# Optimization experiments

Measured on AMD Instinct MI355X. Metric: run time of the kernel, lower is better.

Reference implementation:

```python
import jax, jax.numpy as jnp
import numpy as np

B, T, HID, NH = 8, 4096, 768, 12
HD = HID // NH          # 64
WIN = 128 // 2          # half window = 64 (local_attention=128)
BLK = 64                # block size == half window
THETA = 10000.0         # local_rope_theta
ATTN_SCALING = 1.0      # default rope type


def setup_inputs() -> dict:
    key = jax.random.key(0)
    k1, k2, k3 = jax.random.split(key, 3)
    hidden_states = jax.random.normal(k1, (B, T, HID), jnp.float32)
    attention_mask = jnp.ones((B, T), jnp.bool_)
    Wqkv = jax.random.normal(k2, (3 * HID, HID), jnp.float32) * 0.02
    Wo = jax.random.normal(k3, (HID, HID), jnp.float32) * 0.02
    return {"hidden_states": hidden_states, "attention_mask": attention_mask,
            "Wqkv": Wqkv, "Wo": Wo}


def _rope(x):
    # x: [B, T, NH, HD]; interleaved-pair complex rotation (pairs = reshape(HD//2, 2))
    pos = jnp.arange(T, dtype=jnp.float32)
    inv_freq = 1.0 / (THETA ** (jnp.arange(0, HD, 2, dtype=jnp.float32) / HD))  # [HD/2]
    ang = pos[:, None] * inv_freq[None, :]                 # [T, HD/2]
    cos = jnp.cos(ang)[None, :, None, :]
    sin = jnp.sin(ang)[None, :, None, :]
    pairs = x.reshape(x.shape[:-1] + (HD // 2, 2))
    a, b = pairs[..., 0], pairs[..., 1]
    ra = a * cos - b * sin
    rb = a * sin + b * cos
    return (jnp.stack([ra, rb], axis=-1).reshape(x.shape)) * ATTN_SCALING


def reference(hidden_states, attention_mask, Wqkv, Wo):
    # fused QKV projection (no bias: attention_bias=False)
    qkv = hidden_states @ Wqkv.T                            # [B, T, 3*HID]
    qkv = qkv.reshape(B, T, 3, NH, HD)
    q, k, v = qkv[:, :, 0], qkv[:, :, 1], qkv[:, :, 2]      # [B, T, NH, HD]
    q = _rope(q)
    k = _rope(k)

    # Blocked sliding-window attention: block = 64, each query block attends
    # key blocks {i-1, i, i+1}; exact +/-64 band enforced by mask.
    nb = T // BLK
    pad = [(0, 0), (BLK, BLK), (0, 0), (0, 0)]
    kp = jnp.pad(k, pad)
    vp = jnp.pad(v, pad)
    kb = kp.reshape(B, nb + 2, BLK, NH, HD)
    vb = vp.reshape(B, nb + 2, BLK, NH, HD)
    knb = jnp.concatenate([kb[:, :-2], kb[:, 1:-1], kb[:, 2:]], axis=2)  # [B, nb, 3*BLK, NH, HD]
    vnb = jnp.concatenate([vb[:, :-2], vb[:, 1:-1], vb[:, 2:]], axis=2)
    qb = q.reshape(B, nb, BLK, NH, HD)

    scores = jnp.einsum('bnqhd,bnkhd->bhnqk', qb, knb) / jnp.sqrt(jnp.float32(HD))
    band = jnp.abs(BLK + jnp.arange(BLK)[:, None] - jnp.arange(3 * BLK)[None, :]) <= WIN  # [BLK, 3*BLK]
    mp = jnp.pad(attention_mask.astype(jnp.bool_), [(0, 0), (BLK, BLK)])
    mb = mp.reshape(B, nb + 2, BLK)
    mnb = jnp.concatenate([mb[:, :-2], mb[:, 1:-1], mb[:, 2:]], axis=2)  # [B, nb, 3*BLK]
    mask = band[None, None, None] & mnb[:, None, :, None, :]
    scores = jnp.where(mask, scores, -jnp.inf)
    probs = jax.nn.softmax(scores, axis=-1)
    out = jnp.einsum('bhnqk,bnkhd->bnqhd', probs, vnb)      # [B, nb, BLK, NH, HD]
    out = out.reshape(B, T, HID)
    return out @ Wo.T
```

## Files before the change

kernel.cpp:

```cpp
#include <hip/hip_runtime.h>
#include <hip/hip_bf16.h>

#define T_SEQ 4096
#define NH 12

typedef __bf16 bf16x8 __attribute__((ext_vector_type(8)));
typedef float f32x4 __attribute__((ext_vector_type(4)));
typedef unsigned int uint32;

__device__ __forceinline__ void gload_lds16(const void* g, void* lds) {
    __builtin_amdgcn_global_load_lds((const __attribute__((address_space(1))) void*)g,
                                     (__attribute__((address_space(3))) void*)lds,
                                     16, 0, 0);
}

__device__ __forceinline__ f32x4 mfma16(bf16x8 a, bf16x8 b, f32x4 c) {
    return __builtin_amdgcn_mfma_f32_16x16x32_bf16(a, b, c, 0, 0, 0);
}

__device__ __forceinline__ void store_out(__hip_bfloat16* p, float v) { *p = __float2bfloat16(v); }
__device__ __forceinline__ void store_out(float* p, float v) { *p = v; }

__global__ __launch_bounds__(256) void f32_to_bf16_kernel(const float* __restrict__ src,
                                                          __hip_bfloat16* __restrict__ dst,
                                                          long n8) {
    long i = (long)blockIdx.x * 256 + threadIdx.x;
    if (i >= n8) return;
    float4 a = *(const float4*)(src + i * 8);
    float4 b = *(const float4*)(src + i * 8 + 4);
    __hip_bfloat16 o[8];
    o[0] = __float2bfloat16(a.x); o[1] = __float2bfloat16(a.y);
    o[2] = __float2bfloat16(a.z); o[3] = __float2bfloat16(a.w);
    o[4] = __float2bfloat16(b.x); o[5] = __float2bfloat16(b.y);
    o[6] = __float2bfloat16(b.z); o[7] = __float2bfloat16(b.w);
    *(uint4*)(dst + i * 8) = *(uint4*)o;
}

__global__ void rope_table_kernel(float2* __restrict__ tab) {
    int idx = blockIdx.x * 256 + threadIdx.x;
    int tpos = idx >> 5, i = idx & 31;
    float invf = powf(10000.0f, -(2.0f * i) / 64.0f);
    float ang = (float)tpos * invf;
    tab[idx] = make_float2((float)cos((double)ang), (float)sin((double)ang));
}


#define PHASE(BB, MH, NH, SKIND, SKT, DOSTAGE)                                            \
    do {                                                                                  \
        bf16x8 af[4][2], bq[2][2];                                                        \
        _Pragma("unroll")                                                                 \
        for (int m2 = 0; m2 < 4; ++m2)                                                    \
            _Pragma("unroll")                                                             \
            for (int ks = 0; ks < 2; ++ks) {                                              \
                const int row = wr * 128 + ((MH) * 4 + m2) * 16 + li;                     \
                af[m2][ks] = *(const bf16x8*)((char*)&As[BB][0] + row * 128 +             \
                                              (((ks * 4 + g) ^ (row & 7)) << 4));         \
            }                                                                             \
        _Pragma("unroll")                                                                 \
        for (int n2 = 0; n2 < 2; ++n2)                                                    \
            _Pragma("unroll")                                                             \
            for (int ks = 0; ks < 2; ++ks) {                                              \
                const int row = wc * 64 + ((NH) * 2 + n2) * 16 + li;                      \
                bq[n2][ks] = *(const bf16x8*)((char*)&Bs[BB][0] + row * 128 +             \
                                              (((ks * 4 + g) ^ (row & 7)) << 4));         \
            }                                                                             \
        if (DOSTAGE) STAGE_HT((SKIND), (SKT));                                            \
        __builtin_amdgcn_sched_barrier(0);                                                \
        __builtin_amdgcn_s_barrier();                                                     \
        __builtin_amdgcn_s_setprio(1);                                                    \
        _Pragma("unroll")                                                                 \
        for (int m2 = 0; m2 < 4; ++m2)                                                    \
            _Pragma("unroll")                                                             \
            for (int n2 = 0; n2 < 2; ++n2)                                                \
                _Pragma("unroll")                                                         \
                for (int ks = 0; ks < 2; ++ks)                                            \
                    acc[(MH) * 4 + m2][(NH) * 2 + n2] =                                   \
                        mfma16(af[m2][ks], bq[n2][ks], acc[(MH) * 4 + m2][(NH) * 2 + n2]);\
        __builtin_amdgcn_s_setprio(0);                                                    \
        __builtin_amdgcn_sched_barrier(0);                                                \
    } while (0)

template <typename OutT>
__global__ __launch_bounds__(512) void gemm8p(const __hip_bfloat16* __restrict__ A,
                                              const __hip_bfloat16* __restrict__ Bw,
                                              OutT* __restrict__ C,
                                              int M, int N, int K, int nbn) {
    __shared__ __align__(16) __hip_bfloat16 As[2][256 * 64];
    __shared__ __align__(16) __hip_bfloat16 Bs[2][256 * 64];

    const int tid = threadIdx.x;
    const int w = tid >> 6, l = tid & 63;
    const int g = l >> 4, li = l & 15;
    const int wr = w >> 2, wc = w & 3;

    const int cpx = gridDim.x >> 3;
    const int bid = blockIdx.x;
    const int swz = (bid & 7) * cpx + (bid >> 3);
    const int bm = swz / nbn, bn = swz % nbn;

    const long abase = (long)bm * 256 * K;
    const long bbase = (long)bn * 256 * K;
    const int NT = K >> 6;

    auto STAGE_HT = [&](int kind, int kt) {
        const int sb = kt & 1;
        const int k0 = kt << 6;
#pragma unroll
        for (int i = 0; i < 2; ++i) {
            const int ci = i * 512 + tid;
            const int ir = ci >> 3;
            const int ch = ci & 7;
            const int ir0 = (i * 512 + (tid & ~63)) >> 3;
            int row, row0;
            if (kind < 2) {
                row  = (ir & 63) + ((ir >> 6) << 7) + ((kind & 1) << 6);
                row0 = (ir0 & 63) + ((ir0 >> 6) << 7) + ((kind & 1) << 6);
            } else {
                row  = (ir & 31) + ((ir >> 5) << 6) + ((kind & 1) << 5);
                row0 = (ir0 & 31) + ((ir0 >> 5) << 6) + ((kind & 1) << 5);
            }
            const int sch = ch ^ (row & 7);
            if (kind < 2)
                gload_lds16(A + abase + (long)row * K + k0 + sch * 8,
                            (char*)&As[sb][0] + (size_t)row0 * 128);
            else
                gload_lds16(Bw + bbase + (long)row * K + k0 + sch * 8,
                            (char*)&Bs[sb][0] + (size_t)row0 * 128);
        }
    };

    f32x4 acc[8][4] = {};

    STAGE_HT(0, 0); STAGE_HT(2, 0); STAGE_HT(1, 0); STAGE_HT(3, 0);
    STAGE_HT(2, 1); STAGE_HT(0, 1);
    asm volatile("s_waitcnt vmcnt(4)" ::: "memory");
    __builtin_amdgcn_s_barrier();

    for (int j = 0; j < NT; ++j) {
        const int bb = j & 1;
        PHASE(bb, 0, 0, 1, j + 1, j + 1 < NT);
        __builtin_amdgcn_s_barrier();
        PHASE(bb, 1, 0, 3, j + 1, j + 1 < NT);
        __builtin_amdgcn_s_barrier();
        PHASE(bb, 0, 1, 2, j + 2, j + 2 < NT);
        __builtin_amdgcn_s_barrier();
        PHASE(bb, 1, 1, 0, j + 2, j + 2 < NT);
        if (j + 1 < NT) {
            if (j + 2 < NT) asm volatile("s_waitcnt vmcnt(4)" ::: "memory");
            else            asm volatile("s_waitcnt vmcnt(0)" ::: "memory");
        }
        __builtin_amdgcn_s_barrier();
    }

#pragma unroll
    for (int mi = 0; mi < 8; ++mi)
#pragma unroll
        for (int ni = 0; ni < 4; ++ni)
#pragma unroll
            for (int r = 0; r < 4; ++r) {
                long row = (long)bm * 256 + wr * 128 + mi * 16 + g * 4 + r;
                int col = bn * 256 + wc * 64 + ni * 16 + li;
                store_out(&C[row * (long)N + col], acc[mi][ni][r]);
            }
}

__global__ __launch_bounds__(256) void attn_kernel(const __hip_bfloat16* __restrict__ qkv,
                                                   __hip_bfloat16* __restrict__ attn_out,
                                                   const float2* __restrict__ tab) {
    __shared__ __align__(16) char smem[51200];
    __hip_bfloat16* Qs = (__hip_bfloat16*)smem;
    __hip_bfloat16* Ks = (__hip_bfloat16*)(smem + 9216);
    __hip_bfloat16* Ps = (__hip_bfloat16*)smem;
    __hip_bfloat16* Vs = (__hip_bfloat16*)(smem + 25600);

    const int tid = threadIdx.x;
    const int w = tid >> 6, l = tid & 63;
    const int g = l >> 4, li = l & 15;
    const int mw = w * 16;

    const int bid = blockIdx.x;
    const int n = bid & 63;
    const int bh = bid >> 6;
    const int b = bh / NH, h = bh % NH;

    const long tokq0 = (long)b * T_SEQ + n * 64;
    const long rowbase = (long)b * T_SEQ;

#pragma unroll
    for (int i = 0; i < 2; ++i) {
        int seg = i * 256 + tid;
        int row = seg >> 3, c = (seg & 7) * 8;
        uint4 v = *(const uint4*)&qkv[(tokq0 + row) * 2304 + h * 64 + c];
        __hip_bfloat16 tmp[8], outv[8];
        *(uint4*)tmp = v;
        const int tpos = n * 64 + row;
#pragma unroll
        for (int j = 0; j < 4; ++j) {
            float2 cs = tab[tpos * 32 + (c >> 1) + j];
            float a = __bfloat162float(tmp[2 * j]), bb = __bfloat162float(tmp[2 * j + 1]);
            outv[2 * j]     = __float2bfloat16(a * cs.x - bb * cs.y);
            outv[2 * j + 1] = __float2bfloat16(a * cs.y + bb * cs.x);
        }
        *(uint4*)&Qs[row * 72 + c] = *(uint4*)outv;
    }
#pragma unroll
    for (int i = 0; i < 6; ++i) {
        int seg = i * 256 + tid;
        int row = seg >> 3, c = (seg & 7) * 8;
        int tk = n * 64 - 64 + row;
        tk = tk < 0 ? 0 : (tk > T_SEQ - 1 ? T_SEQ - 1 : tk);
        uint4 v = *(const uint4*)&qkv[(rowbase + tk) * 2304 + 768 + h * 64 + c];
        __hip_bfloat16 tmp[8], outv[8];
        *(uint4*)tmp = v;
#pragma unroll
        for (int j = 0; j < 4; ++j) {
            float2 cs = tab[tk * 32 + (c >> 1) + j];
            float a = __bfloat162float(tmp[2 * j]), bb = __bfloat162float(tmp[2 * j + 1]);
            outv[2 * j]     = __float2bfloat16(a * cs.x - bb * cs.y);
            outv[2 * j + 1] = __float2bfloat16(a * cs.y + bb * cs.x);
        }
        *(uint4*)&Ks[row * 72 + c] = *(uint4*)outv;
    }
    __syncthreads();

    f32x4 s[12] = {};
#pragma unroll
    for (int kk = 0; kk < 64; kk += 32) {
        bf16x8 aq = *(const bf16x8*)&Qs[(mw + li) * 72 + kk + g * 8];
#pragma unroll
        for (int ni = 0; ni < 12; ++ni) {
            bf16x8 bk = *(const bf16x8*)&Ks[(ni * 16 + li) * 72 + kk + g * 8];
            s[ni] = mfma16(aq, bk, s[ni]);
        }
    }

#pragma unroll
    for (int r = 0; r < 4; ++r) {
        int q = mw + g * 4 + r;
        float mx = -1e30f;
#pragma unroll
        for (int ni = 0; ni < 12; ++ni) {
            int k = ni * 16 + li;
            int kpos = n * 64 - 64 + k;
            bool valid = (k >= q) && (k <= q + 128) && (kpos >= 0) && (kpos < T_SEQ);
            float v = valid ? s[ni][r] * 0.125f : -1e30f;
            s[ni][r] = v;
            mx = fmaxf(mx, v);
        }
#pragma unroll
        for (int m = 1; m < 16; m <<= 1) mx = fmaxf(mx, __shfl_xor(mx, m, 64));
        float sum = 0.f;
#pragma unroll
        for (int ni = 0; ni < 12; ++ni) {
            float e = __expf(s[ni][r] - mx);
            s[ni][r] = e;
            sum += e;
        }
#pragma unroll
        for (int m = 1; m < 16; m <<= 1) sum += __shfl_xor(sum, m, 64);
        float inv = 1.0f / sum;
#pragma unroll
        for (int ni = 0; ni < 12; ++ni) s[ni][r] *= inv;
    }
    __syncthreads();

#pragma unroll
    for (int r = 0; r < 4; ++r) {
        int q = mw + g * 4 + r;
#pragma unroll
        for (int ni = 0; ni < 12; ++ni)
            Ps[q * 200 + ni * 16 + li] = __float2bfloat16(s[ni][r]);
    }
#pragma unroll
    for (int i = 0; i < 6; ++i) {
        int seg = i * 256 + tid;
        int row = seg >> 3, c = (seg & 7) * 8;
        int tk = n * 64 - 64 + row;
        tk = tk < 0 ? 0 : (tk > T_SEQ - 1 ? T_SEQ - 1 : tk);
        uint4 v = *(const uint4*)&qkv[(rowbase + tk) * 2304 + 1536 + h * 64 + c];
        __hip_bfloat16 tmp[8];
        *(uint4*)tmp = v;
#pragma unroll
        for (int j = 0; j < 8; ++j) Vs[(c + j) * 200 + row] = tmp[j];
    }
    __syncthreads();

    f32x4 o[4] = {};
#pragma unroll
    for (int kk = 0; kk < 192; kk += 32) {
        bf16x8 ap = *(const bf16x8*)&Ps[(mw + li) * 200 + kk + g * 8];
#pragma unroll
        for (int ni = 0; ni < 4; ++ni) {
            bf16x8 bv = *(const bf16x8*)&Vs[(ni * 16 + li) * 200 + kk + g * 8];
            o[ni] = mfma16(ap, bv, o[ni]);
        }
    }
#pragma unroll
    for (int ni = 0; ni < 4; ++ni)
#pragma unroll
        for (int r = 0; r < 4; ++r) {
            int q = mw + g * 4 + r;
            attn_out[(tokq0 + q) * 768 + h * 64 + ni * 16 + li] = __float2bfloat16(o[ni][r]);
        }
}

extern "C" void kernel_launch(void* const* d_in, const int* in_sizes, int n_in,
                              void* d_out, int out_size, void* d_ws, size_t ws_size,
                              hipStream_t stream) {
    const float* hidden = (const float*)d_in[0];
    const float* Wqkv = (const float*)d_in[2];
    const float* Wo   = (const float*)d_in[3];
    float* out = (float*)d_out;

    char* ws = (char*)d_ws;
    __hip_bfloat16* qkv     = (__hip_bfloat16*)ws;
    __hip_bfloat16* abuf    = (__hip_bfloat16*)(ws + 150994944L);
    __hip_bfloat16* wqkv_bf = (__hip_bfloat16*)(ws + 201326592L);
    __hip_bfloat16* wo_bf   = (__hip_bfloat16*)(ws + 204865536L);
    float2*         tab     = (float2*)(ws + 206045184L);

    f32_to_bf16_kernel<<<12288, 256, 0, stream>>>(hidden, abuf, 3145728);
    f32_to_bf16_kernel<<<864, 256, 0, stream>>>(Wqkv, wqkv_bf, 221184);
    f32_to_bf16_kernel<<<288, 256, 0, stream>>>(Wo, wo_bf, 73728);
    rope_table_kernel<<<512, 256, 0, stream>>>(tab);

    gemm8p<__hip_bfloat16><<<1152, 512, 0, stream>>>(abuf, wqkv_bf, qkv, 32768, 2304, 768, 9);
    attn_kernel<<<6144, 256, 0, stream>>>(qkv, abuf, tab);
    gemm8p<float><<<384, 512, 0, stream>>>(abuf, wo_bf, out, 32768, 768, 768, 3);
}
```

Before: 349.7 us.

## Reorder GEMM sub-tile phases to reuse A/B fragments and cut LDS reads

```diff
diff --git a/kernel.cpp b/kernel.cpp
--- a/kernel.cpp
+++ b/kernel.cpp
@@ -45,25 +45,28 @@
 }
 
 
-#define PHASE(BB, MH, NH, SKIND, SKT, DOSTAGE)                                            \
+#define PHASE(BB, MH, NHQ, LOADA, LOADB, SKIND, SKT, DOSTAGE)                             \
     do {                                                                                  \
-        bf16x8 af[4][2], bq[2][2];                                                        \
-        _Pragma("unroll")                                                                 \
-        for (int m2 = 0; m2 < 4; ++m2)                                                    \
+        if (LOADA) {                                                                      \
             _Pragma("unroll")                                                             \
-            for (int ks = 0; ks < 2; ++ks) {                                              \
-                const int row = wr * 128 + ((MH) * 4 + m2) * 16 + li;                     \
-                af[m2][ks] = *(const bf16x8*)((char*)&As[BB][0] + row * 128 +             \
-                                              (((ks * 4 + g) ^ (row & 7)) << 4));         \
-            }                                                                             \
-        _Pragma("unroll")                                                                 \
-        for (int n2 = 0; n2 < 2; ++n2)                                                    \
+            for (int m2 = 0; m2 < 4; ++m2)                                                \
+                _Pragma("unroll")                                                         \
+                for (int ks = 0; ks < 2; ++ks) {                                          \
+                    const int row = wr * 128 + ((MH) * 4 + m2) * 16 + li;                 \
+                    af[m2][ks] = *(const bf16x8*)((char*)&As[BB][0] + row * 128 +         \
+                                                  (((ks * 4 + g) ^ (row & 7)) << 4));     \
+                }                                                                         \
+        }                                                                                 \
+        if (LOADB) {                                                                      \
             _Pragma("unroll")                                                             \
-            for (int ks = 0; ks < 2; ++ks) {                                              \
-                const int row = wc * 64 + ((NH) * 2 + n2) * 16 + li;                      \
-                bq[n2][ks] = *(const bf16x8*)((char*)&Bs[BB][0] + row * 128 +             \
-                                              (((ks * 4 + g) ^ (row & 7)) << 4));         \
-            }                                                                             \
+            for (int n2 = 0; n2 < 2; ++n2)                                                \
+                _Pragma("unroll")                                                         \
+                for (int ks = 0; ks < 2; ++ks) {                                          \
+                    const int row = wc * 64 + ((NHQ) * 2 + n2) * 16 + li;                 \
+                    bq[n2][ks] = *(const bf16x8*)((char*)&Bs[BB][0] + row * 128 +         \
+                                                  (((ks * 4 + g) ^ (row & 7)) << 4));     \
+                }                                                                         \
+        }                                                                                 \
         if (DOSTAGE) STAGE_HT((SKIND), (SKT));                                            \
         __builtin_amdgcn_sched_barrier(0);                                                \
         __builtin_amdgcn_s_barrier();                                                     \
@@ -74,10 +77,11 @@
             for (int n2 = 0; n2 < 2; ++n2)                                                \
                 _Pragma("unroll")                                                         \
                 for (int ks = 0; ks < 2; ++ks)                                            \
-                    acc[(MH) * 4 + m2][(NH) * 2 + n2] =                                   \
-                        mfma16(af[m2][ks], bq[n2][ks], acc[(MH) * 4 + m2][(NH) * 2 + n2]);\
+                    acc[(MH) * 4 + m2][(NHQ) * 2 + n2] =                                  \
+                        mfma16(af[m2][ks], bq[n2][ks], acc[(MH) * 4 + m2][(NHQ) * 2 + n2]);\
         __builtin_amdgcn_s_setprio(0);                                                    \
         __builtin_amdgcn_sched_barrier(0);                                                \
+        __builtin_amdgcn_s_barrier();                                                     \
     } while (0)
 
 template <typename OutT>
@@ -130,25 +134,21 @@
     };
 
     f32x4 acc[8][4] = {};
-
-    STAGE_HT(0, 0); STAGE_HT(2, 0); STAGE_HT(1, 0); STAGE_HT(3, 0);
-    STAGE_HT(2, 1); STAGE_HT(0, 1);
+    bf16x8 af[4][2], bq[2][2];
+
+    STAGE_HT(0, 0); STAGE_HT(3, 0); STAGE_HT(1, 0); STAGE_HT(2, 0);
+    STAGE_HT(0, 1); STAGE_HT(3, 1);
     asm volatile("s_waitcnt vmcnt(4)" ::: "memory");
     __builtin_amdgcn_s_barrier();
 
     for (int j = 0; j < NT; ++j) {
         const int bb = j & 1;
-        PHASE(bb, 0, 0, 1, j + 1, j + 1 < NT);
-        __builtin_amdgcn_s_barrier();
-        PHASE(bb, 1, 0, 3, j + 1, j + 1 < NT);
-        __builtin_amdgcn_s_barrier();
-        PHASE(bb, 0, 1, 2, j + 2, j + 2 < NT);
-        __builtin_amdgcn_s_barrier();
-        PHASE(bb, 1, 1, 0, j + 2, j + 2 < NT);
-        if (j + 1 < NT) {
-            if (j + 2 < NT) asm volatile("s_waitcnt vmcnt(4)" ::: "memory");
-            else            asm volatile("s_waitcnt vmcnt(0)" ::: "memory");
-        }
+        PHASE(bb, 0, 0, 1, 1, 1, j + 1, j + 1 < NT);
+        PHASE(bb, 0, 1, 0, 1, 2, j + 1, j + 1 < NT);
+        PHASE(bb, 1, 1, 1, 0, 0, j + 2, j + 2 < NT);
+        PHASE(bb, 1, 0, 0, 1, 3, j + 2, j + 2 < NT);
+        if (j + 2 < NT)      asm volatile("s_waitcnt vmcnt(4)" ::: "memory");
+        else if (j + 1 < NT) asm volatile("s_waitcnt vmcnt(0)" ::: "memory");
         __builtin_amdgcn_s_barrier();
     }
 
```

Result: faster. 331.4 us (-5.2%).
